# Performance work log

Measured on AMD Instinct MI355X. Metric: run time of the kernel, lower is better.

The kernel has to match this reference:

```python
import jax, jax.numpy as jnp
import numpy as np

ALPHA = 1.0   # init alpha=1 -> temporal (TDI) term has zero weight
GAMMA = 0.01  # soft-min temperature
INF = 1e9     # finite stand-in for +inf boundary of the DP matrix


def setup_inputs() -> dict:
    key = jax.random.key(0)
    k1, k2 = jax.random.split(key)
    B, N, F = 64, 512, 1
    return {
        "input": jax.random.normal(k1, (B, N, F), dtype=jnp.float32),
        "target": jax.random.normal(k2, (B, N, F), dtype=jnp.float32),
    }


def _soft_dtw(D, gamma):
    """Batched soft-DTW value via anti-diagonal wavefront scan.

    D: (B, n, n) cost matrix. Returns (B,) soft-DTW values R[n, n].
    Recursion: R[i,j] = D[i-1,j-1] + softmin_gamma(R[i-1,j-1], R[i-1,j], R[i,j-1]).
    """
    B, n, _ = D.shape
    ii = jnp.arange(n + 1)           # row index i of diagonal entries
    ic = jnp.clip(ii - 1, 0, n - 1)  # clipped cost-row index (masked below)
    inf_row = jnp.full((B, n + 1), INF, D.dtype)
    diag_d0 = inf_row.at[:, 0].set(0.0)  # R[0,0]=0, rest inf
    diag_d1 = inf_row                    # R[1,0]=R[0,1]=inf
    pad_col = jnp.full((B, 1), INF, D.dtype)

    def step(carry, d):
        r2, r1 = carry  # diagonals d-2, d-1, indexed by i in [0, n]
        jj = d - ii
        jc = jnp.clip(jj - 1, 0, n - 1)
        dvals = D[:, ic, jc]  # (B, n+1) costs along diagonal d
        r2s = jnp.concatenate([pad_col, r2[:, :-1]], axis=1)  # R[i-1, j-1]
        r1s = jnp.concatenate([pad_col, r1[:, :-1]], axis=1)  # R[i-1, j]
        # softmin_gamma(a,b,c) = -gamma * logsumexp(-[a,b,c]/gamma)
        cand = jnp.stack([-r2s, -r1s, -r1], axis=0) / gamma
        smin = -gamma * jax.nn.logsumexp(cand, axis=0)
        valid = (ii >= 1) & (ii <= n) & (jj >= 1) & (jj <= n)
        new = jnp.where(valid[None, :], dvals + smin, INF)
        return (r1, new), None

    (_, last), _ = jax.lax.scan(step, (diag_d0, diag_d1), jnp.arange(2, 2 * n + 1))
    return last[:, n]  # R[n, n] per batch element


def reference(input, target):
    # derivative DILATE: operate on first differences of the series
    dx = input[:, 1:, :] - input[:, :-1, :]   # (B, n, F), n = N-1
    dy = target[:, 1:, :] - target[:, :-1, :]
    # pairwise squared-Euclidean cost D[b, i, j] = ||dy_i - dx_j||^2
    D = jnp.sum((dy[:, :, None, :] - dx[:, None, :, :]) ** 2, axis=-1)
    loss_shape = jnp.mean(_soft_dtw(D, GAMMA))
    # DILATE = alpha * loss_shape + (1 - alpha) * loss_temporal; alpha == 1 here,
    # so the TDI (temporal) term has zero weight and is omitted.
    return ALPHA * loss_shape
```

## Files before the change

kernel.cpp:

```cpp
#include <hip/hip_runtime.h>
#include <math.h>


#define INF_F 1000000000.0f

typedef float v4f __attribute__((ext_vector_type(4)));

__device__ __forceinline__ float dpp_shr1_inj(float x, float oldv){
  int r = __builtin_amdgcn_update_dpp(__float_as_int(oldv), __float_as_int(x),
                                      0x138 , 0xf, 0xf, false);
  return __int_as_float(r);
}
__device__ __forceinline__ float min3f(float a, float b, float c){
  float d;
  asm("v_min3_f32 %0, %1, %2, %3" : "=v"(d) : "v"(a), "v"(b), "v"(c));
  return d;
}
#define PINF(v) asm volatile("" : "+v"(v))

#define LOADW(P, B2) { const float2* _p = dxe2 + (B2); \
  float2 a0=_p[0],a1=_p[1],a2=_p[2],a3=_p[3],a4=_p[4],a5=_p[5],a6=_p[6],a7=_p[7]; \
  float2 a8=_p[8],a9=_p[9],a10=_p[10],a11=_p[11],a12=_p[12],a13=_p[13]; \
  float2 a14=_p[14],a15=_p[15],a16=_p[16]; \
  P##0=a0.x;  P##1=a0.y;  P##2=a1.x;  P##3=a1.y;  P##4=a2.x;  P##5=a2.y; \
  P##6=a3.x;  P##7=a3.y;  P##8=a4.x;  P##9=a4.y;  P##10=a5.x; P##11=a5.y; \
  P##12=a6.x; P##13=a6.y; P##14=a7.x; P##15=a7.y; P##16=a8.x; P##17=a8.y; \
  P##18=a9.x; P##19=a9.y; P##20=a10.x;P##21=a10.y;P##22=a11.x;P##23=a11.y; \
  P##24=a12.x;P##25=a12.y;P##26=a13.x;P##27=a13.y;P##28=a14.x;P##29=a14.y; \
  P##30=a15.x;P##31=a15.y;P##32=a16.x;P##33=a16.y; }

#define PINW(P) { PINF(P##0); PINF(P##1); PINF(P##2); PINF(P##3); PINF(P##4); \
  PINF(P##5); PINF(P##6); PINF(P##7); PINF(P##8); PINF(P##9); PINF(P##10); \
  PINF(P##11); PINF(P##12); PINF(P##13); PINF(P##14); PINF(P##15); PINF(P##16); \
  PINF(P##17); PINF(P##18); PINF(P##19); PINF(P##20); PINF(P##21); PINF(P##22); \
  PINF(P##23); PINF(P##24); PINF(P##25); PINF(P##26); PINF(P##27); PINF(P##28); \
  PINF(P##29); PINF(P##30); PINF(P##31); PINF(P##32); PINF(P##33); }

#define STEP2(K, MB, XLO, XHI) { \
  float sh1 = dpp_shr1_inj(r1_hi, (MB)); \
  float uL  = dy_lo - (XLO); \
  float uH  = dy_hi - (XHI); \
  float nv_hi = fmaf(uH, uH, min3f(r2_lo, r1_lo, r1_hi)); \
  float nv_lo = fmaf(uL, uL, min3f(SH2, sh1, r1_lo)); \
  pb##K = nv_hi; \
  if ((K) == 28) { if (cc == 31) ans = nv_hi; } \
  SH2 = sh1; r2_lo = r1_lo; r1_lo = nv_lo; r1_hi = nv_hi; }

#define CHUNK(C, XU, XP) { \
  const int cc = (C); \
  if (w > 0) { \
    while (__hip_atomic_load(&flagz[w-1], __ATOMIC_ACQUIRE, \
                             __HIP_MEMORY_SCOPE_WORKGROUP) <= cc) { \
      __builtin_amdgcn_s_sleep(1); \
    } \
    const v4f* Mr = (const v4f*)&Mbx[w][32*cc]; \
    q0 = Mr[0]; q1 = Mr[1]; q2 = Mr[2]; q3 = Mr[3]; \
    q4 = Mr[4]; q5 = Mr[5]; q6 = Mr[6]; q7 = Mr[7]; \
    m32v = Mbx[w][32*cc+32]; \
    PINF(q0); PINF(q1); PINF(q2); PINF(q3); \
    PINF(q4); PINF(q5); PINF(q6); PINF(q7); PINF(m32v); \
  } \
  PINW(XU); \
  LOADW(XP, 257 + 16*(cc+1) - t); \
  asm volatile("" ::: "memory"); \
  STEP2(0,  q0.y,  XU##1,  XU##0 ) STEP2(1,  q0.z,  XU##2,  XU##1 ) \
  STEP2(2,  q0.w,  XU##3,  XU##2 ) STEP2(3,  q1.x,  XU##4,  XU##3 ) \
  STEP2(4,  q1.y,  XU##5,  XU##4 ) STEP2(5,  q1.z,  XU##6,  XU##5 ) \
  STEP2(6,  q1.w,  XU##7,  XU##6 ) STEP2(7,  q2.x,  XU##8,  XU##7 ) \
  STEP2(8,  q2.y,  XU##9,  XU##8 ) STEP2(9,  q2.z,  XU##10, XU##9 ) \
  STEP2(10, q2.w,  XU##11, XU##10) STEP2(11, q3.x,  XU##12, XU##11) \
  STEP2(12, q3.y,  XU##13, XU##12) STEP2(13, q3.z,  XU##14, XU##13) \
  STEP2(14, q3.w,  XU##15, XU##14) STEP2(15, q4.x,  XU##16, XU##15) \
  STEP2(16, q4.y,  XU##17, XU##16) STEP2(17, q4.z,  XU##18, XU##17) \
  STEP2(18, q4.w,  XU##19, XU##18) STEP2(19, q5.x,  XU##20, XU##19) \
  STEP2(20, q5.y,  XU##21, XU##20) STEP2(21, q5.z,  XU##22, XU##21) \
  STEP2(22, q5.w,  XU##23, XU##22) STEP2(23, q6.x,  XU##24, XU##23) \
  STEP2(24, q6.y,  XU##25, XU##24) STEP2(25, q6.z,  XU##26, XU##25) \
  STEP2(26, q6.w,  XU##27, XU##26) STEP2(27, q7.x,  XU##28, XU##27) \
  STEP2(28, q7.y,  XU##29, XU##28) STEP2(29, q7.z,  XU##30, XU##29) \
  STEP2(30, q7.w,  XU##31, XU##30) STEP2(31, m32v,  XU##32, XU##31) \
  if (w < 3) { \
    if (lane == 63) { \
      float2* Pd = (float2*)&Mbx[w+1][32*cc+2]; \
      Pd[0]  = make_float2(pb0,  pb1);  Pd[1]  = make_float2(pb2,  pb3); \
      Pd[2]  = make_float2(pb4,  pb5);  Pd[3]  = make_float2(pb6,  pb7); \
      Pd[4]  = make_float2(pb8,  pb9);  Pd[5]  = make_float2(pb10, pb11); \
      Pd[6]  = make_float2(pb12, pb13); Pd[7]  = make_float2(pb14, pb15); \
      Pd[8]  = make_float2(pb16, pb17); Pd[9]  = make_float2(pb18, pb19); \
      Pd[10] = make_float2(pb20, pb21); Pd[11] = make_float2(pb22, pb23); \
      Pd[12] = make_float2(pb24, pb25); Pd[13] = make_float2(pb26, pb27); \
      Pd[14] = make_float2(pb28, pb29); Pd[15] = make_float2(pb30, pb31); \
    } \
    __hip_atomic_store(&flagz[w], cc+1, __ATOMIC_RELEASE, \
                       __HIP_MEMORY_SCOPE_WORKGROUP); \
  } }

__global__ __launch_bounds__(256, 1)
void sdtw_kernel(const float* __restrict__ input,
                 const float* __restrict__ target,
                 float* __restrict__ out) {
  const int b = blockIdx.x;
  const int t = threadIdx.x;
  const int w = t >> 6;
  const int lane = t & 63;

  __shared__ __align__(8) float dxe[1576];
  __shared__ __align__(16) float Mbx[4][1040];
  __shared__ int flagz[4];

  const float* __restrict__ inp = input + b * 512;
  const float* __restrict__ tgt = target + b * 512;

  for (int idx = t; idx < 1576; idx += 256) {
    float v = 0.0f;
    if (idx >= 514 && idx <= 1024) v = inp[idx - 513] - inp[idx - 514];
    dxe[idx] = v;
  }
  for (int k2 = t; k2 < 4 * 1040; k2 += 256) (&Mbx[0][0])[k2] = INF_F;
  if (t < 4) flagz[t] = 0;

  float dy_lo = (t >= 1) ? (tgt[2*t] - tgt[2*t - 1]) : 0.0f;
  float dy_hi = tgt[2*t + 1] - tgt[2*t];

  float r1_lo = INF_F, r1_hi = INF_F;
  float r2_lo = (t == 0) ? 0.0f : INF_F;
  float SH2   = INF_F;

  v4f q0 = {INF_F, INF_F, INF_F, INF_F};
  v4f q1 = q0, q2 = q0, q3 = q0, q4 = q0, q5 = q0, q6 = q0, q7 = q0;
  float m32v = INF_F;
  float pb0,  pb1,  pb2,  pb3,  pb4,  pb5,  pb6,  pb7;
  float pb8,  pb9,  pb10, pb11, pb12, pb13, pb14, pb15;
  float pb16, pb17, pb18, pb19, pb20, pb21, pb22, pb23;
  float pb24, pb25, pb26, pb27, pb28, pb29, pb30, pb31;
  float xa0,xa1,xa2,xa3,xa4,xa5,xa6,xa7,xa8,xa9,xa10,xa11,xa12,xa13,xa14,xa15;
  float xa16,xa17,xa18,xa19,xa20,xa21,xa22,xa23,xa24,xa25,xa26,xa27,xa28,xa29;
  float xa30,xa31,xa32,xa33;
  float xb0,xb1,xb2,xb3,xb4,xb5,xb6,xb7,xb8,xb9,xb10,xb11,xb12,xb13,xb14,xb15;
  float xb16,xb17,xb18,xb19,xb20,xb21,xb22,xb23,xb24,xb25,xb26,xb27,xb28,xb29;
  float xb30,xb31,xb32,xb33;

  float ans = INF_F;
  const float2* dxe2 = (const float2*)dxe;

  __syncthreads();

  LOADW(xa, 257 - t);

#pragma unroll 1
  for (int c = 0; c < 32; c += 2) {
    CHUNK(c,     xa, xb)
    CHUNK(c + 1, xb, xa)
  }

  if (w == 3 && lane == 63) {
    atomicAdd(out, ans * (1.0f / 64.0f));
  }
}

extern "C" void kernel_launch(void* const* d_in, const int* in_sizes, int n_in,
                              void* d_out, int out_size, void* d_ws, size_t ws_size,
                              hipStream_t stream) {
  const float* input  = (const float*)d_in[0];
  const float* target = (const float*)d_in[1];
  float* out = (float*)d_out;

  hipMemsetAsync(out, 0, sizeof(float), stream);
  sdtw_kernel<<<64, 256, 0, stream>>>(input, target, out);
}
```

Before: 85.57 us.

## Collapse four-wave pipelined wavefront into one wave with 8 rows per lane

```diff
diff --git a/kernel.cpp b/kernel.cpp
--- a/kernel.cpp
+++ b/kernel.cpp
@@ -3,8 +3,6 @@
 
 
 #define INF_F 1000000000.0f
-
-typedef float v4f __attribute__((ext_vector_type(4)));
 
 __device__ __forceinline__ float dpp_shr1_inj(float x, float oldv){
   int r = __builtin_amdgcn_update_dpp(__float_as_int(oldv), __float_as_int(x),
@@ -16,136 +14,126 @@
   asm("v_min3_f32 %0, %1, %2, %3" : "=v"(d) : "v"(a), "v"(b), "v"(c));
   return d;
 }
-#define PINF(v) asm volatile("" : "+v"(v))
 
-#define LOADW(P, B2) { const float2* _p = dxe2 + (B2); \
+#define LOADW40(P, FB) { const float2* _p = dxw + (FB); \
   float2 a0=_p[0],a1=_p[1],a2=_p[2],a3=_p[3],a4=_p[4],a5=_p[5],a6=_p[6],a7=_p[7]; \
   float2 a8=_p[8],a9=_p[9],a10=_p[10],a11=_p[11],a12=_p[12],a13=_p[13]; \
-  float2 a14=_p[14],a15=_p[15],a16=_p[16]; \
+  float2 a14=_p[14],a15=_p[15],a16=_p[16],a17=_p[17],a18=_p[18],a19=_p[19]; \
   P##0=a0.x;  P##1=a0.y;  P##2=a1.x;  P##3=a1.y;  P##4=a2.x;  P##5=a2.y; \
   P##6=a3.x;  P##7=a3.y;  P##8=a4.x;  P##9=a4.y;  P##10=a5.x; P##11=a5.y; \
   P##12=a6.x; P##13=a6.y; P##14=a7.x; P##15=a7.y; P##16=a8.x; P##17=a8.y; \
   P##18=a9.x; P##19=a9.y; P##20=a10.x;P##21=a10.y;P##22=a11.x;P##23=a11.y; \
   P##24=a12.x;P##25=a12.y;P##26=a13.x;P##27=a13.y;P##28=a14.x;P##29=a14.y; \
-  P##30=a15.x;P##31=a15.y;P##32=a16.x;P##33=a16.y; }
+  P##30=a15.x;P##31=a15.y;P##32=a16.x;P##33=a16.y;P##34=a17.x;P##35=a17.y; \
+  P##36=a18.x;P##37=a18.y;P##38=a19.x;P##39=a19.y; }
 
-#define PINW(P) { PINF(P##0); PINF(P##1); PINF(P##2); PINF(P##3); PINF(P##4); \
-  PINF(P##5); PINF(P##6); PINF(P##7); PINF(P##8); PINF(P##9); PINF(P##10); \
-  PINF(P##11); PINF(P##12); PINF(P##13); PINF(P##14); PINF(P##15); PINF(P##16); \
-  PINF(P##17); PINF(P##18); PINF(P##19); PINF(P##20); PINF(P##21); PINF(P##22); \
-  PINF(P##23); PINF(P##24); PINF(P##25); PINF(P##26); PINF(P##27); PINF(P##28); \
-  PINF(P##29); PINF(P##30); PINF(P##31); PINF(P##32); PINF(P##33); }
-
-#define STEP2(K, MB, XLO, XHI) { \
-  float sh1 = dpp_shr1_inj(r1_hi, (MB)); \
-  float uL  = dy_lo - (XLO); \
-  float uH  = dy_hi - (XHI); \
-  float nv_hi = fmaf(uH, uH, min3f(r2_lo, r1_lo, r1_hi)); \
-  float nv_lo = fmaf(uL, uL, min3f(SH2, sh1, r1_lo)); \
-  pb##K = nv_hi; \
-  if ((K) == 28) { if (cc == 31) ans = nv_hi; } \
-  SH2 = sh1; r2_lo = r1_lo; r1_lo = nv_lo; r1_hi = nv_hi; }
+#define STEP8(K, W0, W1, W2, W3, W4, W5, W6, W7) { \
+  float sh1 = dpp_shr1_inj(r1_7, INF_F); \
+  float u0 = dy0 - (W0); float u1 = dy1 - (W1); \
+  float u2 = dy2 - (W2); float u3 = dy3 - (W3); \
+  float u4 = dy4 - (W4); float u5 = dy5 - (W5); \
+  float u6 = dy6 - (W6); float u7 = dy7 - (W7); \
+  float nv0 = fmaf(u0, u0, min3f(SH2,  sh1,  r1_0)); \
+  float nv1 = fmaf(u1, u1, min3f(r2_0, r1_0, r1_1)); \
+  float nv2 = fmaf(u2, u2, min3f(r2_1, r1_1, r1_2)); \
+  float nv3 = fmaf(u3, u3, min3f(r2_2, r1_2, r1_3)); \
+  float nv4 = fmaf(u4, u4, min3f(r2_3, r1_3, r1_4)); \
+  float nv5 = fmaf(u5, u5, min3f(r2_4, r1_4, r1_5)); \
+  float nv6 = fmaf(u6, u6, min3f(r2_5, r1_5, r1_6)); \
+  float nv7 = fmaf(u7, u7, min3f(r2_6, r1_6, r1_7)); \
+  if ((K) == 28) { if (cc == 31) ans = nv7; } \
+  SH2 = sh1; \
+  r2_0 = r1_0; r2_1 = r1_1; r2_2 = r1_2; r2_3 = r1_3; \
+  r2_4 = r1_4; r2_5 = r1_5; r2_6 = r1_6; \
+  r1_0 = nv0; r1_1 = nv1; r1_2 = nv2; r1_3 = nv3; \
+  r1_4 = nv4; r1_5 = nv5; r1_6 = nv6; r1_7 = nv7; }
 
 #define CHUNK(C, XU, XP) { \
   const int cc = (C); \
-  if (w > 0) { \
-    while (__hip_atomic_load(&flagz[w-1], __ATOMIC_ACQUIRE, \
-                             __HIP_MEMORY_SCOPE_WORKGROUP) <= cc) { \
-      __builtin_amdgcn_s_sleep(1); \
-    } \
-    const v4f* Mr = (const v4f*)&Mbx[w][32*cc]; \
-    q0 = Mr[0]; q1 = Mr[1]; q2 = Mr[2]; q3 = Mr[3]; \
-    q4 = Mr[4]; q5 = Mr[5]; q6 = Mr[6]; q7 = Mr[7]; \
-    m32v = Mbx[w][32*cc+32]; \
-    PINF(q0); PINF(q1); PINF(q2); PINF(q3); \
-    PINF(q4); PINF(q5); PINF(q6); PINF(q7); PINF(m32v); \
-  } \
-  PINW(XU); \
-  LOADW(XP, 257 + 16*(cc+1) - t); \
-  asm volatile("" ::: "memory"); \
-  STEP2(0,  q0.y,  XU##1,  XU##0 ) STEP2(1,  q0.z,  XU##2,  XU##1 ) \
-  STEP2(2,  q0.w,  XU##3,  XU##2 ) STEP2(3,  q1.x,  XU##4,  XU##3 ) \
-  STEP2(4,  q1.y,  XU##5,  XU##4 ) STEP2(5,  q1.z,  XU##6,  XU##5 ) \
-  STEP2(6,  q1.w,  XU##7,  XU##6 ) STEP2(7,  q2.x,  XU##8,  XU##7 ) \
-  STEP2(8,  q2.y,  XU##9,  XU##8 ) STEP2(9,  q2.z,  XU##10, XU##9 ) \
-  STEP2(10, q2.w,  XU##11, XU##10) STEP2(11, q3.x,  XU##12, XU##11) \
-  STEP2(12, q3.y,  XU##13, XU##12) STEP2(13, q3.z,  XU##14, XU##13) \
-  STEP2(14, q3.w,  XU##15, XU##14) STEP2(15, q4.x,  XU##16, XU##15) \
-  STEP2(16, q4.y,  XU##17, XU##16) STEP2(17, q4.z,  XU##18, XU##17) \
-  STEP2(18, q4.w,  XU##19, XU##18) STEP2(19, q5.x,  XU##20, XU##19) \
-  STEP2(20, q5.y,  XU##21, XU##20) STEP2(21, q5.z,  XU##22, XU##21) \
-  STEP2(22, q5.w,  XU##23, XU##22) STEP2(23, q6.x,  XU##24, XU##23) \
-  STEP2(24, q6.y,  XU##25, XU##24) STEP2(25, q6.z,  XU##26, XU##25) \
-  STEP2(26, q6.w,  XU##27, XU##26) STEP2(27, q7.x,  XU##28, XU##27) \
-  STEP2(28, q7.y,  XU##29, XU##28) STEP2(29, q7.z,  XU##30, XU##29) \
-  STEP2(30, q7.w,  XU##31, XU##30) STEP2(31, m32v,  XU##32, XU##31) \
-  if (w < 3) { \
-    if (lane == 63) { \
-      float2* Pd = (float2*)&Mbx[w+1][32*cc+2]; \
-      Pd[0]  = make_float2(pb0,  pb1);  Pd[1]  = make_float2(pb2,  pb3); \
-      Pd[2]  = make_float2(pb4,  pb5);  Pd[3]  = make_float2(pb6,  pb7); \
-      Pd[4]  = make_float2(pb8,  pb9);  Pd[5]  = make_float2(pb10, pb11); \
-      Pd[6]  = make_float2(pb12, pb13); Pd[7]  = make_float2(pb14, pb15); \
-      Pd[8]  = make_float2(pb16, pb17); Pd[9]  = make_float2(pb18, pb19); \
-      Pd[10] = make_float2(pb20, pb21); Pd[11] = make_float2(pb22, pb23); \
-      Pd[12] = make_float2(pb24, pb25); Pd[13] = make_float2(pb26, pb27); \
-      Pd[14] = make_float2(pb28, pb29); Pd[15] = make_float2(pb30, pb31); \
-    } \
-    __hip_atomic_store(&flagz[w], cc+1, __ATOMIC_RELEASE, \
-                       __HIP_MEMORY_SCOPE_WORKGROUP); \
-  } }
+  if (cc < 31) { LOADW40(XP, fb0 + 16 * (cc + 1)); } \
+  STEP8(0,  XU##7,  XU##6,  XU##5,  XU##4,  XU##3,  XU##2,  XU##1,  XU##0 ) \
+  STEP8(1,  XU##8,  XU##7,  XU##6,  XU##5,  XU##4,  XU##3,  XU##2,  XU##1 ) \
+  STEP8(2,  XU##9,  XU##8,  XU##7,  XU##6,  XU##5,  XU##4,  XU##3,  XU##2 ) \
+  STEP8(3,  XU##10, XU##9,  XU##8,  XU##7,  XU##6,  XU##5,  XU##4,  XU##3 ) \
+  STEP8(4,  XU##11, XU##10, XU##9,  XU##8,  XU##7,  XU##6,  XU##5,  XU##4 ) \
+  STEP8(5,  XU##12, XU##11, XU##10, XU##9,  XU##8,  XU##7,  XU##6,  XU##5 ) \
+  STEP8(6,  XU##13, XU##12, XU##11, XU##10, XU##9,  XU##8,  XU##7,  XU##6 ) \
+  STEP8(7,  XU##14, XU##13, XU##12, XU##11, XU##10, XU##9,  XU##8,  XU##7 ) \
+  STEP8(8,  XU##15, XU##14, XU##13, XU##12, XU##11, XU##10, XU##9,  XU##8 ) \
+  STEP8(9,  XU##16, XU##15, XU##14, XU##13, XU##12, XU##11, XU##10, XU##9 ) \
+  STEP8(10, XU##17, XU##16, XU##15, XU##14, XU##13, XU##12, XU##11, XU##10) \
+  STEP8(11, XU##18, XU##17, XU##16, XU##15, XU##14, XU##13, XU##12, XU##11) \
+  STEP8(12, XU##19, XU##18, XU##17, XU##16, XU##15, XU##14, XU##13, XU##12) \
+  STEP8(13, XU##20, XU##19, XU##18, XU##17, XU##16, XU##15, XU##14, XU##13) \
+  STEP8(14, XU##21, XU##20, XU##19, XU##18, XU##17, XU##16, XU##15, XU##14) \
+  STEP8(15, XU##22, XU##21, XU##20, XU##19, XU##18, XU##17, XU##16, XU##15) \
+  STEP8(16, XU##23, XU##22, XU##21, XU##20, XU##19, XU##18, XU##17, XU##16) \
+  STEP8(17, XU##24, XU##23, XU##22, XU##21, XU##20, XU##19, XU##18, XU##17) \
+  STEP8(18, XU##25, XU##24, XU##23, XU##22, XU##21, XU##20, XU##19, XU##18) \
+  STEP8(19, XU##26, XU##25, XU##24, XU##23, XU##22, XU##21, XU##20, XU##19) \
+  STEP8(20, XU##27, XU##26, XU##25, XU##24, XU##23, XU##22, XU##21, XU##20) \
+  STEP8(21, XU##28, XU##27, XU##26, XU##25, XU##24, XU##23, XU##22, XU##21) \
+  STEP8(22, XU##29, XU##28, XU##27, XU##26, XU##25, XU##24, XU##23, XU##22) \
+  STEP8(23, XU##30, XU##29, XU##28, XU##27, XU##26, XU##25, XU##24, XU##23) \
+  STEP8(24, XU##31, XU##30, XU##29, XU##28, XU##27, XU##26, XU##25, XU##24) \
+  STEP8(25, XU##32, XU##31, XU##30, XU##29, XU##28, XU##27, XU##26, XU##25) \
+  STEP8(26, XU##33, XU##32, XU##31, XU##30, XU##29, XU##28, XU##27, XU##26) \
+  STEP8(27, XU##34, XU##33, XU##32, XU##31, XU##30, XU##29, XU##28, XU##27) \
+  STEP8(28, XU##35, XU##34, XU##33, XU##32, XU##31, XU##30, XU##29, XU##28) \
+  STEP8(29, XU##36, XU##35, XU##34, XU##33, XU##32, XU##31, XU##30, XU##29) \
+  STEP8(30, XU##37, XU##36, XU##35, XU##34, XU##33, XU##32, XU##31, XU##30) \
+  STEP8(31, XU##38, XU##37, XU##36, XU##35, XU##34, XU##33, XU##32, XU##31) }
 
-__global__ __launch_bounds__(256, 1)
+__global__ __launch_bounds__(64, 1)
 void sdtw_kernel(const float* __restrict__ input,
                  const float* __restrict__ target,
                  float* __restrict__ out) {
   const int b = blockIdx.x;
   const int t = threadIdx.x;
-  const int w = t >> 6;
-  const int lane = t & 63;
 
-  __shared__ __align__(8) float dxe[1576];
-  __shared__ __align__(16) float Mbx[4][1040];
-  __shared__ int flagz[4];
+  __shared__ __align__(8) float dxe[4 * 1546];
 
   const float* __restrict__ inp = input + b * 512;
   const float* __restrict__ tgt = target + b * 512;
 
-  for (int idx = t; idx < 1576; idx += 256) {
-    float v = 0.0f;
-    if (idx >= 514 && idx <= 1024) v = inp[idx - 513] - inp[idx - 514];
-    dxe[idx] = v;
-  }
-  for (int k2 = t; k2 < 4 * 1040; k2 += 256) (&Mbx[0][0])[k2] = INF_F;
-  if (t < 4) flagz[t] = 0;
+  for (int rr = 0; rr < 4; ++rr)
+    for (int i = t; i < 1546; i += 64) {
+      float v = 0.0f;
+      if (i >= 512 && i <= 1022) v = inp[i - 511] - inp[i - 512];
+      dxe[rr * 1546 + i] = v;
+    }
 
-  float dy_lo = (t >= 1) ? (tgt[2*t] - tgt[2*t - 1]) : 0.0f;
-  float dy_hi = tgt[2*t + 1] - tgt[2*t];
+  const int rb = 8 * t;
+  float dy0 = (t == 0) ? 0.0f : tgt[rb]     - tgt[rb - 1];
+  float dy1 = tgt[rb + 1] - tgt[rb];
+  float dy2 = tgt[rb + 2] - tgt[rb + 1];
+  float dy3 = tgt[rb + 3] - tgt[rb + 2];
+  float dy4 = tgt[rb + 4] - tgt[rb + 3];
+  float dy5 = tgt[rb + 5] - tgt[rb + 4];
+  float dy6 = tgt[rb + 6] - tgt[rb + 5];
+  float dy7 = tgt[rb + 7] - tgt[rb + 6];
 
-  float r1_lo = INF_F, r1_hi = INF_F;
-  float r2_lo = (t == 0) ? 0.0f : INF_F;
-  float SH2   = INF_F;
+  float r1_0 = INF_F, r1_1 = INF_F, r1_2 = INF_F, r1_3 = INF_F;
+  float r1_4 = INF_F, r1_5 = INF_F, r1_6 = INF_F, r1_7 = INF_F;
+  float r2_0 = (t == 0) ? 0.0f : INF_F;
+  float r2_1 = INF_F, r2_2 = INF_F, r2_3 = INF_F;
+  float r2_4 = INF_F, r2_5 = INF_F, r2_6 = INF_F;
+  float SH2 = INF_F;
+  float ans = INF_F;
 
-  v4f q0 = {INF_F, INF_F, INF_F, INF_F};
-  v4f q1 = q0, q2 = q0, q3 = q0, q4 = q0, q5 = q0, q6 = q0, q7 = q0;
-  float m32v = INF_F;
-  float pb0,  pb1,  pb2,  pb3,  pb4,  pb5,  pb6,  pb7;
-  float pb8,  pb9,  pb10, pb11, pb12, pb13, pb14, pb15;
-  float pb16, pb17, pb18, pb19, pb20, pb21, pb22, pb23;
-  float pb24, pb25, pb26, pb27, pb28, pb29, pb30, pb31;
   float xa0,xa1,xa2,xa3,xa4,xa5,xa6,xa7,xa8,xa9,xa10,xa11,xa12,xa13,xa14,xa15;
   float xa16,xa17,xa18,xa19,xa20,xa21,xa22,xa23,xa24,xa25,xa26,xa27,xa28,xa29;
-  float xa30,xa31,xa32,xa33;
+  float xa30,xa31,xa32,xa33,xa34,xa35,xa36,xa37,xa38,xa39;
   float xb0,xb1,xb2,xb3,xb4,xb5,xb6,xb7,xb8,xb9,xb10,xb11,xb12,xb13,xb14,xb15;
   float xb16,xb17,xb18,xb19,xb20,xb21,xb22,xb23,xb24,xb25,xb26,xb27,xb28,xb29;
-  float xb30,xb31,xb32,xb33;
+  float xb30,xb31,xb32,xb33,xb34,xb35,xb36,xb37,xb38,xb39;
 
-  float ans = INF_F;
-  const float2* dxe2 = (const float2*)dxe;
+  const float2* dxw = ((const float2*)dxe) + 773 * ((t >> 2) & 3);
+  const int fb0 = 253 - 4 * t;
 
   __syncthreads();
 
-  LOADW(xa, 257 - t);
+  LOADW40(xa, fb0);
 
 #pragma unroll 1
   for (int c = 0; c < 32; c += 2) {
@@ -153,7 +141,7 @@
     CHUNK(c + 1, xb, xa)
   }
 
-  if (w == 3 && lane == 63) {
+  if (t == 63) {
     atomicAdd(out, ans * (1.0f / 64.0f));
   }
 }
@@ -166,5 +154,5 @@
   float* out = (float*)d_out;
 
   hipMemsetAsync(out, 0, sizeof(float), stream);
-  sdtw_kernel<<<64, 256, 0, stream>>>(input, target, out);
+  sdtw_kernel<<<64, 64, 0, stream>>>(input, target, out);
 }
```

New measurement: 108.5 us. 26.8% more time.
